# Optimization experiments

Hardware: AMD Instinct MI355X
Metric: run time of the kernel (lower is better)

Reference implementation:

```python
import jax, jax.numpy as jnp
import numpy as np

EPS = 1e-12  # matches torch F.normalize eps


def _l2norm(t):
    n = jnp.linalg.norm(t, axis=-1, keepdims=True)
    return t / jnp.maximum(n, EPS)


def setup_inputs() -> dict:
    key = jax.random.key(0)
    ks = jax.random.split(key, 10)
    B, N, C = 2, 2048, 384
    nH, hd = 12, 32
    inp = {
        "x": jax.random.normal(ks[0], (B, N, C), jnp.float32),
        "q_w": jax.random.normal(ks[1], (C, C), jnp.float32) * 0.02,
        "q_b": jax.random.normal(ks[2], (C,), jnp.float32) * 0.02,
        "kv_w": jax.random.normal(ks[3], (2 * C, C), jnp.float32) * 0.02,
        "kv_b": jax.random.normal(ks[4], (2 * C,), jnp.float32) * 0.02,
        "query_embedding": jax.random.normal(ks[5], (nH, 1, hd), jnp.float32) * 0.02,
        # init of temperature in torch: log(exp(1/0.24) - 1)
        "temperature": jnp.full((nH, 1, 1), float(np.log(np.exp(1.0 / 0.24) - 1.0)), jnp.float32),
        "pos_bias": jax.random.normal(ks[7], (nH, N), jnp.float32) * 0.0004,
        "proj_w": jax.random.normal(ks[8], (C, C), jnp.float32) * 0.02,
        "proj_b": jax.random.normal(ks[9], (C,), jnp.float32) * 0.02,
        "D": 8, "H": 16, "W": 16,
    }
    return inp


def reference(x, q_w, q_b, kv_w, kv_b, query_embedding, temperature, pos_bias, proj_w, proj_b, D, H, W):
    B, N, C = x.shape
    nH, hd = query_embedding.shape[0], query_embedding.shape[2]
    assert N == D * H * W
    # q projection -> [B, nH, N, hd], cosine-normalized
    q = (x @ q_w.T + q_b).reshape(B, N, nH, hd).transpose(0, 2, 1, 3)
    q = _l2norm(q)
    # additive query embedding, softplus temperature, seq-length (log N) scale
    scale = jax.nn.softplus(temperature) * jnp.float32(np.log(N))  # [nH,1,1]
    q = (q + query_embedding[None]) * scale[None]
    # kv projection
    kv = x @ kv_w.T + kv_b  # [B, N, 2C]
    k, v = kv[..., :C], kv[..., C:]
    k = _l2norm(k.reshape(B, N, nH, hd).transpose(0, 2, 1, 3))
    v = v.reshape(B, N, nH, hd).transpose(0, 2, 1, 3)
    # scores with per-head learned positional bias over keys
    attn = jnp.einsum("bhqd,bhkd->bhqk", q, k) + pos_bias[None, :, None, :]
    attn = jax.nn.softmax(attn, axis=-1)
    out = jnp.einsum("bhqk,bhkd->bhqd", attn, v)
    out = out.transpose(0, 2, 1, 3).reshape(B, N, C)
    return out @ proj_w.T + proj_b
```

## Files before the change

kernel.cpp:

```cpp
#include <hip/hip_runtime.h>

#define LOG2E 1.4426950408889634f

typedef __bf16 bf16x8 __attribute__((ext_vector_type(8)));
typedef short s16x4 __attribute__((ext_vector_type(4)));
typedef float f32x4 __attribute__((ext_vector_type(4)));

#define BB 2
#define NN 2048
#define CC 384
#define NH 12
#define HD 32

__device__ __forceinline__ unsigned short f2bf(float f) {
  __bf16 h = (__bf16)f;
  return __builtin_bit_cast(unsigned short, h);
}

__device__ __forceinline__ bf16x8 ldg_bf8(const unsigned short* p) {
  uint4 v = *reinterpret_cast<const uint4*>(p);
  return __builtin_bit_cast(bf16x8, v);
}

__device__ __forceinline__ float fexp2(float x) {
#if __has_builtin(__builtin_amdgcn_exp2f)
  return __builtin_amdgcn_exp2f(x);
#else
  return exp2f(x);
#endif
}

__device__ __forceinline__ s16x4 pack_bf4(float a, float b, float c, float d) {
#if __has_builtin(__builtin_amdgcn_cvt_pk_bf16_f32)
  auto lo = __builtin_amdgcn_cvt_pk_bf16_f32(a, b);
  auto hi = __builtin_amdgcn_cvt_pk_bf16_f32(c, d);
  uint2 u = {__builtin_bit_cast(unsigned int, lo),
             __builtin_bit_cast(unsigned int, hi)};
  return __builtin_bit_cast(s16x4, u);
#else
  s16x4 r = {(short)f2bf(a), (short)f2bf(b), (short)f2bf(c), (short)f2bf(d)};
  return r;
#endif
}

typedef __attribute__((address_space(1))) const void gas_void;
typedef __attribute__((address_space(3))) void las_void;
__device__ __forceinline__ void gload_lds16(const void* g, void* l) {
  __builtin_amdgcn_global_load_lds((gas_void*)(unsigned long long)g,
                                   (las_void*)(unsigned long long)l, 16, 0, 0);
}

__device__ __forceinline__ f32x4 mfma32(bf16x8 a, bf16x8 b, f32x4 c) {
  return __builtin_amdgcn_mfma_f32_16x16x32_bf16(a, b, c, 0, 0, 0);
}

__device__ __forceinline__ f32x4 mfma16(s16x4 a, s16x4 b, f32x4 c) {
#if defined(__HIP_DEVICE_COMPILE__)
#if __has_builtin(__builtin_amdgcn_mfma_f32_16x16x16bf16_1k)
  return __builtin_amdgcn_mfma_f32_16x16x16bf16_1k(a, b, c, 0, 0, 0);
#else
  asm volatile("v_mfma_f32_16x16x16_bf16 %0, %1, %2, %0"
               : "+v"(c) : "v"(a), "v"(b));
  return c;
#endif
#else
  return c;
#endif
}

__global__ __launch_bounds__(256) void prep_kernel(
    const float* __restrict__ x, const float* __restrict__ q_w,
    const float* __restrict__ kv_w, const float* __restrict__ proj_w,
    const float* __restrict__ pos_bias, unsigned short* __restrict__ xb,
    unsigned short* __restrict__ qwb, unsigned short* __restrict__ kvwb,
    unsigned short* __restrict__ pwb, float* __restrict__ bias2) {
  long i = (long)(blockIdx.x * 256 + threadIdx.x) * 8;
  auto cast8 = [&](const float* s, unsigned short* d, long off) {
    float4 a = *reinterpret_cast<const float4*>(s + off);
    float4 b = *reinterpret_cast<const float4*>(s + off + 4);
    s16x4 lo = pack_bf4(a.x, a.y, a.z, a.w);
    s16x4 hi = pack_bf4(b.x, b.y, b.z, b.w);
    uint2 l = __builtin_bit_cast(uint2, lo), h = __builtin_bit_cast(uint2, hi);
    uint4 o = {l.x, l.y, h.x, h.y};
    *reinterpret_cast<uint4*>(d + off) = o;
  };
  if (i < 1572864) { cast8(x, xb, i); return; }
  i -= 1572864;
  if (i < 147456) { cast8(q_w, qwb, i); return; }
  i -= 147456;
  if (i < 294912) { cast8(kv_w, kvwb, i); return; }
  i -= 294912;
  if (i < 147456) { cast8(proj_w, pwb, i); return; }
  i -= 147456;
  float4 a = *reinterpret_cast<const float4*>(pos_bias + i);
  float4 b = *reinterpret_cast<const float4*>(pos_bias + i + 4);
  a.x *= LOG2E; a.y *= LOG2E; a.z *= LOG2E; a.w *= LOG2E;
  b.x *= LOG2E; b.y *= LOG2E; b.z *= LOG2E; b.w *= LOG2E;
  *reinterpret_cast<float4*>(bias2 + i) = a;
  *reinterpret_cast<float4*>(bias2 + i + 4) = b;
}

__global__ __launch_bounds__(256, 4) void gemm_qkv_norm_kernel(
    const unsigned short* __restrict__ xb, const unsigned short* __restrict__ qwb,
    const unsigned short* __restrict__ kvwb, const float* __restrict__ q_b,
    const float* __restrict__ kv_b, const float* __restrict__ qe,
    const float* __restrict__ temperature, unsigned short* __restrict__ Qs,
    unsigned short* __restrict__ Kn, unsigned short* __restrict__ VT) {
  __shared__ alignas(16) char smem[2][20480];
  int wave = threadIdx.x >> 6, lane = threadIdx.x & 63;
  int c = lane & 15, quad = lane >> 4;
  int h = blockIdx.y;
  int m0b = blockIdx.x * 64;
  int cid = wave * 64 + lane;

  auto stage = [&](int buf, int kk) {
    char* base = smem[buf];
#pragma unroll
    for (int j = 0; j < 2; ++j) {
      int chunk = j * 256 + cid;
      int row = chunk >> 3, e = chunk & 7;
      gload_lds16(xb + (long)(m0b + row) * CC + kk + (e ^ (row & 7)) * 8,
                  base + j * 4096 + wave * 1024);
    }
#pragma unroll
    for (int j = 0; j < 3; ++j) {
      int chunk = j * 256 + cid;
      int row = chunk >> 3, e = chunk & 7;
      const unsigned short* src;
      if (row < 32)      src = qwb + (long)(h * 32 + row) * CC;
      else if (row < 64) src = kvwb + (long)(h * 32 + (row - 32)) * CC;
      else               src = kvwb + (long)(CC + h * 32 + (row - 64)) * CC;
      gload_lds16(src + kk + (e ^ (row & 7)) * 8,
                  base + 8192 + j * 4096 + wave * 1024);
    }
  };

  f32x4 acc[6] = {};
  auto compute = [&](int buf) {
    const char* base = smem[buf];
#pragma unroll
    for (int kh = 0; kh < 2; ++kh) {
      int sa = ((kh * 4 + quad) ^ (c & 7)) * 16;
      bf16x8 a = *(const bf16x8*)(base + (wave * 16 + c) * 128 + sa);
#pragma unroll
      for (int t = 0; t < 6; ++t) {
        bf16x8 b = *(const bf16x8*)(base + 8192 + (t * 16 + c) * 128 + sa);
        acc[t] = mfma32(a, b, acc[t]);
      }
    }
  };

  stage(0, 0);
#pragma unroll 1
  for (int s = 0; s < 6; ++s) {
    __syncthreads();
    if (s < 5) stage((s + 1) & 1, (s + 1) * 64);
    compute(s & 1);
  }

  int m0 = m0b + wave * 16;
  float qb0 = q_b[h * 32 + c], qb1 = q_b[h * 32 + 16 + c];
  float kb0 = kv_b[h * 32 + c], kb1 = kv_b[h * 32 + 16 + c];
  float vb0 = kv_b[CC + h * 32 + c], vb1 = kv_b[CC + h * 32 + 16 + c];
  float qe0 = qe[h * HD + c], qe1 = qe[h * HD + 16 + c];
  float sc = log1pf(expf(temperature[h])) * 11.0f;
  int b = m0 >> 11;
  int nb = (m0 & 2047) + quad * 4;
  int pair = b * NH + h;
  unsigned short* qsb = Qs + ((long)pair * NN + nb) * HD;
  unsigned short* knb = Kn + ((long)pair * NN + nb) * HD;
  ushort4 vp0, vp1;
#pragma unroll
  for (int r = 0; r < 4; ++r) {
    float q0 = acc[0][r] + qb0, q1 = acc[1][r] + qb1;
    float k0 = acc[2][r] + kb0, k1 = acc[3][r] + kb1;
    float v0 = acc[4][r] + vb0, v1 = acc[5][r] + vb1;
    float qs = q0 * q0 + q1 * q1, ks = k0 * k0 + k1 * k1;
#pragma unroll
    for (int off = 8; off; off >>= 1) {
      qs += __shfl_xor(qs, off);
      ks += __shfl_xor(ks, off);
    }
    float qi = 1.0f / fmaxf(sqrtf(qs), 1e-12f);
    float ki = 1.0f / fmaxf(sqrtf(ks), 1e-12f);
    qsb[r * HD + c] = f2bf((q0 * qi + qe0) * sc);
    qsb[r * HD + 16 + c] = f2bf((q1 * qi + qe1) * sc);
    knb[r * HD + c] = f2bf(k0 * ki);
    knb[r * HD + 16 + c] = f2bf(k1 * ki);
    ((unsigned short*)&vp0)[r] = f2bf(v0);
    ((unsigned short*)&vp1)[r] = f2bf(v1);
  }
  long vbo = ((long)pair * 64 + (nb >> 5)) * 1024 + (nb & 31);
  *reinterpret_cast<ushort4*>(VT + vbo + c * 32) = vp0;
  *reinterpret_cast<ushort4*>(VT + vbo + (16 + c) * 32) = vp1;
}

__global__ __launch_bounds__(256, 3) void attn_kernel(
    const unsigned short* __restrict__ Qs, const unsigned short* __restrict__ Kn,
    const unsigned short* __restrict__ VT, const float* __restrict__ bias2,
    unsigned short* __restrict__ ao) {
  __shared__ alignas(16) char smem[40960];
  int wave = threadIdx.x >> 6, lane = threadIdx.x & 63;
  int c = lane & 15, quad = lane >> 4;
  int id = blockIdx.x;
  int xcd = id & 7, rr = id >> 3;
  int pair = (rr >> 5) * 8 + xcd;
  int qt = rr & 31;
  int h = pair % NH, b = pair / NH;
  const unsigned short* Qp = Qs + (long)pair * NN * HD;
  const char* Kg0 = (const char*)(Kn + (long)pair * NN * HD) + wave * 32768;
  const char* Vg0 = (const char*)(VT) + ((long)pair * 64 + wave * 16) * 2048;
  const char* bp = (const char*)(bias2 + h * NN);
  int q0 = qt * 64;
  bf16x8 qf0 = ldg_bf8(Qp + (long)(q0 + c) * HD + quad * 8);
  bf16x8 qf1 = ldg_bf8(Qp + (long)(q0 + 16 + c) * HD + quad * 8);
  bf16x8 qf2 = ldg_bf8(Qp + (long)(q0 + 32 + c) * HD + quad * 8);
  bf16x8 qf3 = ldg_bf8(Qp + (long)(q0 + 48 + c) * HD + quad * 8);
  f32x4 o00 = {}, o10 = {}, o01 = {}, o11 = {};
  f32x4 o02 = {}, o12 = {}, o03 = {}, o13 = {};
  f32x4 ro0 = {}, ro1 = {}, ro2 = {}, ro3 = {};
  const s16x4 vone = {(short)0x3F80, (short)0x3F80,
                      (short)0x3F80, (short)0x3F80};

  char* sw = smem + wave * 8192;
  char* biasl = smem + 32768;
  const int koff = (c * 4 + quad) * 16;
  int vd = lane >> 2, ve = lane & 3;
  int ves = ve ^ (vd & 3);

  auto stage = [&](int buf, int i) {
    char* tb = sw + buf * 4096;
    const char* Kg = Kg0 + i * 2048;
    const char* Vg = Vg0 + i * 2048;
#pragma unroll
    for (int j = 0; j < 2; ++j) {
      gload_lds16(Kg + j * 1024 + koff, tb + j * 1024);
      gload_lds16(Vg + (long)(j * 16 + vd) * 64 + ves * 16,
                  tb + 2048 + j * 1024);
    }
  };

#define FRAG_STEP(QF, O0, O1, RO)              \
  {                                            \
    f32x4 s = mfma32(kf, QF, bbv);             \
    float p0 = fexp2(s[0]), p1 = fexp2(s[1]);  \
    float p2 = fexp2(s[2]), p3 = fexp2(s[3]);  \
    s16x4 pf = pack_bf4(p0, p1, p2, p3);       \
    RO = mfma16(vone, pf, RO);                 \
    O0 = mfma16(vlo, pf, O0);                  \
    O1 = mfma16(vhi, pf, O1);                  \
  }

  auto compute = [&](int buf, int i) {
    const char* kb = sw + buf * 4096 + lane * 16;
    const char* vb = sw + buf * 4096 + 2048;
    const char* bl = biasl + wave * 2048 + i * 128 + quad * 16;
#pragma unroll
    for (int t8 = 0; t8 < 2; ++t8) {
      bf16x8 kf = *(const bf16x8*)(kb + t8 * 1024);
      f32x4 bbv = *(const f32x4*)(bl + t8 * 64);
      int sl = ((t8 * 2 + (quad >> 1)) ^ (c & 3)) * 16 + (quad & 1) * 8;
      s16x4 vlo = *(const s16x4*)(vb + c * 64 + sl);
      s16x4 vhi = *(const s16x4*)(vb + 1024 + c * 64 + sl);
      FRAG_STEP(qf0, o00, o10, ro0)
      FRAG_STEP(qf1, o01, o11, ro1)
      FRAG_STEP(qf2, o02, o12, ro2)
      FRAG_STEP(qf3, o03, o13, ro3)
    }
  };
#undef FRAG_STEP

#pragma unroll
  for (int j = 0; j < 2; ++j)
    gload_lds16(bp + j * 4096 + wave * 1024 + lane * 16,
                biasl + j * 4096 + wave * 1024);
  stage(0, 0);
  __syncthreads();

#pragma unroll 1
  for (int i = 0; i < 16; ++i) {
    asm volatile("s_waitcnt lgkmcnt(0)" ::: "memory");
    if (i < 15) {
      stage((i + 1) & 1, i + 1);
      asm volatile("s_waitcnt vmcnt(4)" ::: "memory");
    } else {
      asm volatile("s_waitcnt vmcnt(0)" ::: "memory");
    }
    __builtin_amdgcn_sched_barrier(0);
    compute(i & 1, i);
  }

  __syncthreads();
  float* comb = (float*)smem;
#define PUT(F, O0, O1, RS)                                          \
  {                                                                 \
    float* p = comb + ((F * 4 + wave) * 9) * 64 + lane;             \
    p[0] = O0[0]; p[64] = O0[1]; p[128] = O0[2]; p[192] = O0[3];    \
    p[256] = O1[0]; p[320] = O1[1]; p[384] = O1[2]; p[448] = O1[3]; \
    p[512] = RS;                                                    \
  }
  PUT(0, o00, o10, ro0[0])
  PUT(1, o01, o11, ro1[0])
  PUT(2, o02, o12, ro2[0])
  PUT(3, o03, o13, ro3[0])
#undef PUT
  __syncthreads();
  f32x4 A0 = {}, A1 = {};
  float AR = 0.f;
#pragma unroll
  for (int w2 = 0; w2 < 4; ++w2) {
    const float* p = comb + ((wave * 4 + w2) * 9) * 64 + lane;
    A0[0] += p[0]; A0[1] += p[64]; A0[2] += p[128]; A0[3] += p[192];
    A1[0] += p[256]; A1[1] += p[320]; A1[2] += p[384]; A1[3] += p[448];
    AR += p[512];
  }
  float inv = 1.0f / AR;
  int qr = q0 + wave * 16 + c;
  unsigned short* op = ao + (long)(b * NN + qr) * CC + h * HD + quad * 4;
  ushort4 s0, s1;
#pragma unroll
  for (int r = 0; r < 4; ++r) {
    ((unsigned short*)&s0)[r] = f2bf(A0[r] * inv);
    ((unsigned short*)&s1)[r] = f2bf(A1[r] * inv);
  }
  *reinterpret_cast<ushort4*>(op) = s0;
  *reinterpret_cast<ushort4*>(op + 16) = s1;
}

__global__ __launch_bounds__(256, 4) void proj_kernel(
    const unsigned short* __restrict__ ab, const unsigned short* __restrict__ pwb,
    const float* __restrict__ proj_b, float* __restrict__ out) {
  __shared__ alignas(16) char smem[2][12288];
  int wave = threadIdx.x >> 6, lane = threadIdx.x & 63;
  int c = lane & 15, quad = lane >> 4;
  int m0b = blockIdx.x * 64;
  int n0 = blockIdx.y * 32;
  int cid = wave * 64 + lane;

  auto stage = [&](int buf, int kk) {
    char* base = smem[buf];
#pragma unroll
    for (int j = 0; j < 2; ++j) {
      int chunk = j * 256 + cid;
      int row = chunk >> 3, e = chunk & 7;
      gload_lds16(ab + (long)(m0b + row) * CC + kk + (e ^ (row & 7)) * 8,
                  base + j * 4096 + wave * 1024);
    }
    {
      int row = cid >> 3, e = cid & 7;
      gload_lds16(pwb + (long)(n0 + row) * CC + kk + (e ^ (row & 7)) * 8,
                  base + 8192 + wave * 1024);
    }
  };

  f32x4 acc[2] = {};
  auto compute = [&](int buf) {
    const char* base = smem[buf];
#pragma unroll
    for (int kh = 0; kh < 2; ++kh) {
      int sa = ((kh * 4 + quad) ^ (c & 7)) * 16;
      bf16x8 a = *(const bf16x8*)(base + (wave * 16 + c) * 128 + sa);
#pragma unroll
      for (int t = 0; t < 2; ++t) {
        bf16x8 b = *(const bf16x8*)(base + 8192 + (t * 16 + c) * 128 + sa);
        acc[t] = mfma32(a, b, acc[t]);
      }
    }
  };

  stage(0, 0);
#pragma unroll 1
  for (int s = 0; s < 6; ++s) {
    __syncthreads();
    if (s < 5) stage((s + 1) & 1, (s + 1) * 64);
    compute(s & 1);
  }

  int m0 = m0b + wave * 16;
#pragma unroll
  for (int t = 0; t < 2; ++t) {
    int o = n0 + t * 16 + c;
    float bv = proj_b[o];
#pragma unroll
    for (int r = 0; r < 4; ++r) {
      out[(long)(m0 + quad * 4 + r) * CC + o] = acc[t][r] + bv;
    }
  }
}

extern "C" void kernel_launch(void* const* d_in, const int* in_sizes, int n_in,
                              void* d_out, int out_size, void* d_ws, size_t ws_size,
                              hipStream_t stream) {
  const float* x = (const float*)d_in[0];
  const float* q_w = (const float*)d_in[1];
  const float* q_b = (const float*)d_in[2];
  const float* kv_w = (const float*)d_in[3];
  const float* kv_b = (const float*)d_in[4];
  const float* qe = (const float*)d_in[5];
  const float* temp = (const float*)d_in[6];
  const float* pos_bias = (const float*)d_in[7];
  const float* proj_w = (const float*)d_in[8];
  const float* proj_b = (const float*)d_in[9];
  float* out = (float*)d_out;

  char* ws = (char*)d_ws;
  unsigned short* xb = (unsigned short*)(ws + 0);
  unsigned short* qwb = (unsigned short*)(ws + 3145728);
  unsigned short* kvwb = (unsigned short*)(ws + 3440640);
  unsigned short* pwb = (unsigned short*)(ws + 4030464);
  unsigned short* Qs = (unsigned short*)(ws + 4325376);
  unsigned short* Kn = (unsigned short*)(ws + 7471104);
  unsigned short* VT = (unsigned short*)(ws + 10616832);
  unsigned short* ao = (unsigned short*)(ws + 13762560);
  float* bias2 = (float*)(ws + 16908288);

  prep_kernel<<<1068, 256, 0, stream>>>(x, q_w, kv_w, proj_w, pos_bias, xb, qwb,
                                        kvwb, pwb, bias2);
  gemm_qkv_norm_kernel<<<dim3(64, NH), 256, 0, stream>>>(xb, qwb, kvwb, q_b, kv_b,
                                                         qe, temp, Qs, Kn, VT);
  attn_kernel<<<768, 256, 0, stream>>>(Qs, Kn, VT, bias2, ao);
  proj_kernel<<<dim3(64, 12), 256, 0, stream>>>(ao, pwb, proj_b, out);
}
```

Before: 122.5 us.

## Triple-buffer K/V staging in attention and store positional bias as bf16

```diff
diff --git a/kernel.cpp b/kernel.cpp
--- a/kernel.cpp
+++ b/kernel.cpp
@@ -73,31 +73,26 @@
     const float* __restrict__ kv_w, const float* __restrict__ proj_w,
     const float* __restrict__ pos_bias, unsigned short* __restrict__ xb,
     unsigned short* __restrict__ qwb, unsigned short* __restrict__ kvwb,
-    unsigned short* __restrict__ pwb, float* __restrict__ bias2) {
+    unsigned short* __restrict__ pwb, unsigned short* __restrict__ bias2) {
   long i = (long)(blockIdx.x * 256 + threadIdx.x) * 8;
-  auto cast8 = [&](const float* s, unsigned short* d, long off) {
+  auto cast8 = [&](const float* s, unsigned short* d, long off, float scale) {
     float4 a = *reinterpret_cast<const float4*>(s + off);
     float4 b = *reinterpret_cast<const float4*>(s + off + 4);
-    s16x4 lo = pack_bf4(a.x, a.y, a.z, a.w);
-    s16x4 hi = pack_bf4(b.x, b.y, b.z, b.w);
+    s16x4 lo = pack_bf4(a.x * scale, a.y * scale, a.z * scale, a.w * scale);
+    s16x4 hi = pack_bf4(b.x * scale, b.y * scale, b.z * scale, b.w * scale);
     uint2 l = __builtin_bit_cast(uint2, lo), h = __builtin_bit_cast(uint2, hi);
     uint4 o = {l.x, l.y, h.x, h.y};
     *reinterpret_cast<uint4*>(d + off) = o;
   };
-  if (i < 1572864) { cast8(x, xb, i); return; }
+  if (i < 1572864) { cast8(x, xb, i, 1.0f); return; }
   i -= 1572864;
-  if (i < 147456) { cast8(q_w, qwb, i); return; }
+  if (i < 147456) { cast8(q_w, qwb, i, 1.0f); return; }
   i -= 147456;
-  if (i < 294912) { cast8(kv_w, kvwb, i); return; }
+  if (i < 294912) { cast8(kv_w, kvwb, i, 1.0f); return; }
   i -= 294912;
-  if (i < 147456) { cast8(proj_w, pwb, i); return; }
+  if (i < 147456) { cast8(proj_w, pwb, i, 1.0f); return; }
   i -= 147456;
-  float4 a = *reinterpret_cast<const float4*>(pos_bias + i);
-  float4 b = *reinterpret_cast<const float4*>(pos_bias + i + 4);
-  a.x *= LOG2E; a.y *= LOG2E; a.z *= LOG2E; a.w *= LOG2E;
-  b.x *= LOG2E; b.y *= LOG2E; b.z *= LOG2E; b.w *= LOG2E;
-  *reinterpret_cast<float4*>(bias2 + i) = a;
-  *reinterpret_cast<float4*>(bias2 + i + 4) = b;
+  cast8(pos_bias, bias2, i, LOG2E);
 }
 
 __global__ __launch_bounds__(256, 4) void gemm_qkv_norm_kernel(
@@ -197,9 +192,9 @@
 
 __global__ __launch_bounds__(256, 3) void attn_kernel(
     const unsigned short* __restrict__ Qs, const unsigned short* __restrict__ Kn,
-    const unsigned short* __restrict__ VT, const float* __restrict__ bias2,
+    const unsigned short* __restrict__ VT, const unsigned short* __restrict__ bias2,
     unsigned short* __restrict__ ao) {
-  __shared__ alignas(16) char smem[40960];
+  __shared__ alignas(16) char smem[53248];
   int wave = threadIdx.x >> 6, lane = threadIdx.x & 63;
   int c = lane & 15, quad = lane >> 4;
   int id = blockIdx.x;
@@ -210,7 +205,7 @@
   const unsigned short* Qp = Qs + (long)pair * NN * HD;
   const char* Kg0 = (const char*)(Kn + (long)pair * NN * HD) + wave * 32768;
   const char* Vg0 = (const char*)(VT) + ((long)pair * 64 + wave * 16) * 2048;
-  const char* bp = (const char*)(bias2 + h * NN);
+  const char* bpb = (const char*)(bias2 + h * NN);
   int q0 = qt * 64;
   bf16x8 qf0 = ldg_bf8(Qp + (long)(q0 + c) * HD + quad * 8);
   bf16x8 qf1 = ldg_bf8(Qp + (long)(q0 + 16 + c) * HD + quad * 8);
@@ -222,8 +217,8 @@
   const s16x4 vone = {(short)0x3F80, (short)0x3F80,
                       (short)0x3F80, (short)0x3F80};
 
-  char* sw = smem + wave * 8192;
-  char* biasl = smem + 32768;
+  char* sw = smem + wave * 12288;
+  char* biasl = smem + 49152;
   const int koff = (c * 4 + quad) * 16;
   int vd = lane >> 2, ve = lane & 3;
   int ves = ve ^ (vd & 3);
@@ -254,11 +249,17 @@
   auto compute = [&](int buf, int i) {
     const char* kb = sw + buf * 4096 + lane * 16;
     const char* vb = sw + buf * 4096 + 2048;
-    const char* bl = biasl + wave * 2048 + i * 128 + quad * 16;
+    const char* bl = biasl + wave * 1024 + i * 64 + quad * 8;
 #pragma unroll
     for (int t8 = 0; t8 < 2; ++t8) {
       bf16x8 kf = *(const bf16x8*)(kb + t8 * 1024);
-      f32x4 bbv = *(const f32x4*)(bl + t8 * 64);
+      s16x4 bbp = *(const s16x4*)(bl + t8 * 32);
+      uint2 bu = __builtin_bit_cast(uint2, bbp);
+      f32x4 bbv;
+      bbv[0] = __builtin_bit_cast(float, bu.x << 16);
+      bbv[1] = __builtin_bit_cast(float, bu.x & 0xFFFF0000u);
+      bbv[2] = __builtin_bit_cast(float, bu.y << 16);
+      bbv[3] = __builtin_bit_cast(float, bu.y & 0xFFFF0000u);
       int sl = ((t8 * 2 + (quad >> 1)) ^ (c & 3)) * 16 + (quad & 1) * 8;
       s16x4 vlo = *(const s16x4*)(vb + c * 64 + sl);
       s16x4 vhi = *(const s16x4*)(vb + 1024 + c * 64 + sl);
@@ -270,24 +271,24 @@
   };
 #undef FRAG_STEP
 
-#pragma unroll
-  for (int j = 0; j < 2; ++j)
-    gload_lds16(bp + j * 4096 + wave * 1024 + lane * 16,
-                biasl + j * 4096 + wave * 1024);
+  gload_lds16(bpb + wave * 1024 + lane * 16, biasl + wave * 1024);
   stage(0, 0);
+  stage(1, 1);
   __syncthreads();
 
 #pragma unroll 1
   for (int i = 0; i < 16; ++i) {
     asm volatile("s_waitcnt lgkmcnt(0)" ::: "memory");
-    if (i < 15) {
-      stage((i + 1) & 1, i + 1);
+    if (i < 14) {
+      stage((i + 2) % 3, i + 2);
+      asm volatile("s_waitcnt vmcnt(4)" ::: "memory");
+    } else if (i == 14) {
       asm volatile("s_waitcnt vmcnt(4)" ::: "memory");
     } else {
       asm volatile("s_waitcnt vmcnt(0)" ::: "memory");
     }
     __builtin_amdgcn_sched_barrier(0);
-    compute(i & 1, i);
+    compute(i % 3, i);
   }
 
   __syncthreads();
@@ -412,7 +413,7 @@
   unsigned short* Kn = (unsigned short*)(ws + 7471104);
   unsigned short* VT = (unsigned short*)(ws + 10616832);
   unsigned short* ao = (unsigned short*)(ws + 13762560);
-  float* bias2 = (float*)(ws + 16908288);
+  unsigned short* bias2 = (unsigned short*)(ws + 16908288);
 
   prep_kernel<<<1068, 256, 0, stream>>>(x, q_w, kv_w, proj_w, pos_bias, xb, qwb,
                                         kvwb, pwb, bias2);
```

Measured after the change: 126.2 us. 1.03x slower.
